# Kernel optimization log

Measured on AMD Instinct MI355X. Metric: run time of the kernel, lower is better.

The kernel has to match this reference:

```python
import jax, jax.numpy as jnp
import numpy as np

N, C, K2 = 40000, 128, 9  # active voxels, channels, 3x3 kernel taps
HEAD_OUT = {"hm": 3, "center": 2, "center_z": 1, "dim": 3, "rot": 2}
EPS = 1e-5
INIT_BIAS = -2.66


def setup_inputs() -> dict:
    key = jax.random.key(0)
    ks = jax.random.split(key, 16)
    feats = jax.random.normal(ks[0], (N, C), dtype=jnp.float32)
    # precomputed submanifold-conv neighbor indices (one per kernel tap, all valid)
    nbr_idx = jax.random.randint(ks[1], (N, K2), 0, N, dtype=jnp.int32)
    H = len(HEAD_OUT)
    inp = {"feats": feats, "nbr_idx": nbr_idx}
    # stacked 3x3 SubMConv weights for all heads (kaiming-ish scale)
    inp["W1"] = jax.random.normal(ks[2], (H, K2, C, C), dtype=jnp.float32) * (2.0 / (K2 * C)) ** 0.5
    inp["gamma"] = jnp.ones((H, C), jnp.float32)
    inp["beta"] = jnp.zeros((H, C), jnp.float32)
    for i, (name, oc) in enumerate(HEAD_OUT.items()):
        inp[f"w_{name}"] = jax.random.normal(ks[3 + i], (C, oc), dtype=jnp.float32) * (2.0 / C) ** 0.5
        inp[f"b_{name}"] = (jnp.full((oc,), INIT_BIAS, jnp.float32) if name == "hm"
                             else jnp.zeros((oc,), jnp.float32))
    return inp


def reference(feats, nbr_idx, W1, gamma, beta,
              w_hm, b_hm, w_center, b_center, w_center_z, b_center_z,
              w_dim, b_dim, w_rot, b_rot):
    # SubMConv2d as gather + contraction over kernel taps (shared by all heads)
    gathered = feats[nbr_idx]                       # [N, K2, C]
    y = jnp.einsum('nkc,hkcd->hnd', gathered, W1)   # [H, N, C]
    # BatchNorm1d (training-mode forward: biased batch stats over voxels) + ReLU
    mean = y.mean(axis=1, keepdims=True)
    var = y.var(axis=1, keepdims=True)
    y = jax.nn.relu((y - mean) * jax.lax.rsqrt(var + EPS) * gamma[:, None, :] + beta[:, None, :])
    # per-head 1x1 SubMConv with bias
    heads = [(w_hm, b_hm), (w_center, b_center), (w_center_z, b_center_z),
             (w_dim, b_dim), (w_rot, b_rot)]
    outs = [y[i] @ w + b for i, (w, b) in enumerate(heads)]
    # concat head outputs along channel: [N, 3+2+1+3+2] = [N, 11]
    return jnp.concatenate(outs, axis=-1)
```

## Files before the change

kernel.cpp:

```cpp
#include <hip/hip_runtime.h>
#include <stdint.h>

#define NVOX 40000
#define CCH  128
#define K2   9
#define NH   5
#define TILES 313

typedef __attribute__((ext_vector_type(8))) short bf16x8;
typedef __attribute__((ext_vector_type(4))) float f32x4;

__device__ __forceinline__ unsigned short f2b(float f) {
  union { float f; unsigned int u; } v; v.f = f;
  return (unsigned short)((v.u + 0x7fffu + ((v.u >> 16) & 1u)) >> 16);
}
__device__ __forceinline__ float b2f(unsigned short u) {
  union { unsigned int u; float f; } v; v.u = ((unsigned int)u) << 16;
  return v.f;
}
__device__ __forceinline__ void g2l16(const void* g, void* l) {
  __builtin_amdgcn_global_load_lds(
      (const __attribute__((address_space(1))) unsigned int*)g,
      (__attribute__((address_space(3))) unsigned int*)l, 16, 0, 0);
}
__device__ __forceinline__ int swz(int row, int col) {
  return row * 128 + ((((col >> 3) ^ (row & 15)) << 3) | (col & 7));
}

__global__ void prep(const float4* __restrict__ feats, ushort4* __restrict__ fb,
                     const float* __restrict__ w1, unsigned short* __restrict__ w1t,
                     float* __restrict__ sums) {
  __shared__ unsigned short t[128 * 34];
  int b = blockIdx.x;
  if (b < 5000) {
    int i = b * 256 + threadIdx.x;
    if (i < NVOX * CCH / 4) {
      float4 v = feats[i];
      ushort4 r;
      r.x = f2b(v.x); r.y = f2b(v.y); r.z = f2b(v.z); r.w = f2b(v.w);
      fb[i] = r;
    }
    return;
  }
  if (b == 5180) {
    for (int i = threadIdx.x; i < 2 * NH * CCH; i += 256) sums[i] = 0.f;
    return;
  }
  int bb = b - 5000;
  int tile = bb >> 2;
  int q = bb & 3;
  const float* src = w1 + (size_t)tile * 16384 + q * 32 * 128;
  for (int e = threadIdx.x; e < 4096; e += 256) {
    int c = e >> 7, d = e & 127;
    t[d * 34 + c] = f2b(src[e]);
  }
  __syncthreads();
  unsigned short* dst = w1t + (size_t)tile * 16384 + q * 32;
  for (int e = threadIdx.x; e < 4096; e += 256) {
    int d = e >> 5, c = e & 31;
    dst[d * 128 + c] = t[d * 34 + c];
  }
}

__device__ __forceinline__ void stageB(unsigned short* dstbuf, const unsigned short* wp,
                                       int wave, int lane) {
  int lcol = lane & 15, lrow = lane >> 4;
#pragma unroll
  for (int i = 0; i < 8; ++i) {
    int elem = wave * 4096 + i * 512;
    int row = (elem >> 7) + lrow;
    g2l16(wp + row * 128 + ((lcol ^ (row & 15)) << 3), &dstbuf[elem]);
  }
}

__global__ void __launch_bounds__(256, 2) conv_gemm(
    const unsigned short* __restrict__ fb,
    const int* __restrict__ nbr,
    const unsigned short* __restrict__ w1t,
    unsigned short* __restrict__ yb,
    float* __restrict__ sums)
{
  __shared__ __align__(16) unsigned short Bsb[2][128 * 128];
  __shared__ int idxs[128 * K2];

  const int bid = blockIdx.x;
  const int s = bid / 40;
  const int r = bid % 40;
  const int h = r >> 3;
  const int x = r & 7;
  const int tile = s * 8 + x;
  if (tile >= TILES) return;
  const int n0 = tile * 128;

  const int tid = threadIdx.x;
  const int wave = tid >> 6;
  const int lane = tid & 63;
  const int m = lane & 15;
  const int quad = lane >> 4;

  const unsigned short* wh = w1t + ((size_t)h * K2 << 14);

  stageB(Bsb[0], wh, wave, lane);

  for (int i = tid; i < 128 * K2; i += 256) {
    int rr = i / K2;
    int gn = n0 + rr; if (gn > NVOX - 1) gn = NVOX - 1;
    idxs[i] = nbr[gn * K2 + (i - rr * K2)];
  }
  __syncthreads();

  bf16x8 A[2][2][4];
  {
    int i0 = idxs[(wave * 32 + m) * K2 + 0];
    int i1 = idxs[(wave * 32 + 16 + m) * K2 + 0];
    const unsigned short* p0 = fb + (size_t)i0 * CCH + quad * 8;
    const unsigned short* p1 = fb + (size_t)i1 * CCH + quad * 8;
#pragma unroll
    for (int kc = 0; kc < 4; ++kc) {
      A[0][0][kc] = *(const bf16x8*)(p0 + kc * 32);
      A[0][1][kc] = *(const bf16x8*)(p1 + kc * 32);
    }
  }

  f32x4 acc[2][8] = {};

#pragma unroll
  for (int k = 0; k < K2; ++k) {
    const int par = k & 1;
    if (k + 1 < K2) {
      stageB(Bsb[par ^ 1], wh + ((size_t)(k + 1) << 14), wave, lane);
      int i0 = idxs[(wave * 32 + m) * K2 + k + 1];
      int i1 = idxs[(wave * 32 + 16 + m) * K2 + k + 1];
      const unsigned short* p0 = fb + (size_t)i0 * CCH + quad * 8;
      const unsigned short* p1 = fb + (size_t)i1 * CCH + quad * 8;
#pragma unroll
      for (int kc = 0; kc < 4; ++kc) {
        A[par ^ 1][0][kc] = *(const bf16x8*)(p0 + kc * 32);
        A[par ^ 1][1][kc] = *(const bf16x8*)(p1 + kc * 32);
      }
    }
    const unsigned short* Bcur = Bsb[par];
#pragma unroll
    for (int kc = 0; kc < 4; ++kc) {
      bf16x8 bfr[8];
#pragma unroll
      for (int ni = 0; ni < 8; ++ni)
        bfr[ni] = *(const bf16x8*)&Bcur[(ni * 16 + m) * CCH + (((kc * 4 + quad) ^ m) << 3)];
#pragma unroll
      for (int ni = 0; ni < 8; ++ni) {
        acc[0][ni] = __builtin_amdgcn_mfma_f32_16x16x32_bf16(A[par][0][kc], bfr[ni], acc[0][ni], 0, 0, 0);
        acc[1][ni] = __builtin_amdgcn_mfma_f32_16x16x32_bf16(A[par][1][kc], bfr[ni], acc[1][ni], 0, 0, 0);
      }
    }
    if (k + 1 < K2) {
      asm volatile("s_waitcnt vmcnt(0)" ::: "memory");
      __syncthreads();
    }
  }

  __syncthreads();
  const bool full = (n0 + 128 <= NVOX);
  unsigned short* epi = (unsigned short*)Bsb[0];
  float2* pb = (float2*)Bsb[1];

#pragma unroll
  for (int mi = 0; mi < 2; ++mi)
#pragma unroll
    for (int ni = 0; ni < 8; ++ni)
#pragma unroll
      for (int rr = 0; rr < 4; ++rr) {
        int row = wave * 32 + mi * 16 + quad * 4 + rr;
        int col = ni * 16 + m;
        epi[swz(row, col)] = f2b(acc[mi][ni][rr]);
      }

#pragma unroll
  for (int ni = 0; ni < 8; ++ni) {
    float sm = 0.f, q = 0.f;
#pragma unroll
    for (int mi = 0; mi < 2; ++mi)
#pragma unroll
      for (int rr = 0; rr < 4; ++rr) {
        float v = acc[mi][ni][rr];
        if (!full && n0 + wave * 32 + mi * 16 + quad * 4 + rr >= NVOX) v = 0.f;
        sm += v; q += v * v;
      }
    pb[(ni * 16 + m) * 17 + wave * 4 + quad] = make_float2(sm, q);
  }
  __syncthreads();

  for (int i = tid; i < 2048; i += 256) {
    int row = i >> 4;
    int c = i & 15;
    if (n0 + row < NVOX)
      *(bf16x8*)(yb + ((size_t)h * NVOX + n0 + row) * CCH + c * 8) =
          *(const bf16x8*)&epi[row * 128 + ((c ^ (row & 15)) << 3)];
  }

  if (tid < 128) {
    float sm = 0.f, q = 0.f;
#pragma unroll
    for (int c = 0; c < 16; ++c) {
      float2 p = pb[tid * 17 + c];
      sm += p.x; q += p.y;
    }
    atomicAdd(&sums[h * CCH + tid], sm);
    atomicAdd(&sums[NH * CCH + h * CCH + tid], q);
  }
}

__global__ void finalize_bn(const float* __restrict__ sums, const float* __restrict__ gamma,
                            const float* __restrict__ beta, float* __restrict__ ssb) {
  int h = blockIdx.x, c = threadIdx.x;
  float mean = sums[h * CCH + c] * (1.f / NVOX);
  float var = sums[NH * CCH + h * CCH + c] * (1.f / NVOX) - mean * mean;
  float rstd = rsqrtf(var + 1e-5f);
  float scale = rstd * gamma[h * CCH + c];
  ssb[h * CCH + c] = scale;
  ssb[NH * CCH + h * CCH + c] = beta[h * CCH + c] - mean * scale;
}

__global__ void __launch_bounds__(256) head_fuse(
    const unsigned short* __restrict__ yb, const float* __restrict__ ssb,
    const float* __restrict__ w_hm, const float* __restrict__ b_hm,
    const float* __restrict__ w_ce, const float* __restrict__ b_ce,
    const float* __restrict__ w_cz, const float* __restrict__ b_cz,
    const float* __restrict__ w_dm, const float* __restrict__ b_dm,
    const float* __restrict__ w_rt, const float* __restrict__ b_rt,
    float* __restrict__ out)
{
  __shared__ unsigned short t[64 * 128];
  __shared__ float pbuf[4][64][12];

  const int tid = threadIdx.x;
  const int v0 = blockIdx.x * 64;
  const int vx = tid & 63;
  const int qd = tid >> 6;

  float part[11];
#pragma unroll
  for (int j = 0; j < 11; ++j) part[j] = 0.f;

#pragma unroll
  for (int h = 0; h < NH; ++h) {
    __syncthreads();
#pragma unroll
    for (int i = 0; i < 4; ++i) {
      int idx = i * 256 + tid;
      int row = idx >> 4, c = idx & 15;
      *(bf16x8*)&t[row * 128 + ((c ^ (row & 15)) << 3)] =
          *(const bf16x8*)(yb + ((size_t)h * NVOX + v0 + row) * CCH + c * 8);
    }
    __syncthreads();

    const float* sc = ssb + h * CCH;
    const float* sh = ssb + NH * CCH + h * CCH;
    const float* wp; int oc, off;
    switch (h) {
      case 0: wp = w_hm; oc = 3; off = 0; break;
      case 1: wp = w_ce; oc = 2; off = 3; break;
      case 2: wp = w_cz; oc = 1; off = 5; break;
      case 3: wp = w_dm; oc = 3; off = 6; break;
      default: wp = w_rt; oc = 2; off = 9; break;
    }
#pragma unroll
    for (int qq = 0; qq < 4; ++qq) {
      int q8 = qd * 4 + qq;
      bf16x8 pk = *(const bf16x8*)&t[vx * 128 + ((q8 ^ (vx & 15)) << 3)];
#pragma unroll
      for (int e = 0; e < 8; ++e) {
        int d = q8 * 8 + e;
        float z = fmaf(b2f((unsigned short)pk[e]), sc[d], sh[d]);
        z = fmaxf(z, 0.f);
        const float* wr = wp + d * oc;
        part[off] = fmaf(z, wr[0], part[off]);
        if (oc > 1) part[off + 1] = fmaf(z, wr[1], part[off + 1]);
        if (oc > 2) part[off + 2] = fmaf(z, wr[2], part[off + 2]);
      }
    }
  }

#pragma unroll
  for (int j = 0; j < 11; ++j) pbuf[qd][vx][j] = part[j];
  __syncthreads();
  if (tid < 64) {
    float o[11];
#pragma unroll
    for (int j = 0; j < 11; ++j)
      o[j] = pbuf[0][tid][j] + pbuf[1][tid][j] + pbuf[2][tid][j] + pbuf[3][tid][j];
    o[0] += b_hm[0]; o[1] += b_hm[1]; o[2] += b_hm[2];
    o[3] += b_ce[0]; o[4] += b_ce[1];
    o[5] += b_cz[0];
    o[6] += b_dm[0]; o[7] += b_dm[1]; o[8] += b_dm[2];
    o[9] += b_rt[0]; o[10] += b_rt[1];
    float* op = out + (size_t)(v0 + tid) * 11;
#pragma unroll
    for (int j = 0; j < 11; ++j) op[j] = o[j];
  }
}

extern "C" void kernel_launch(void* const* d_in, const int* in_sizes, int n_in,
                              void* d_out, int out_size, void* d_ws, size_t ws_size,
                              hipStream_t stream) {
  const float* feats = (const float*)d_in[0];
  const int*   nbr   = (const int*)d_in[1];
  const float* W1    = (const float*)d_in[2];
  const float* gamma = (const float*)d_in[3];
  const float* beta  = (const float*)d_in[4];
  const float* w_hm = (const float*)d_in[5];  const float* b_hm = (const float*)d_in[6];
  const float* w_ce = (const float*)d_in[7];  const float* b_ce = (const float*)d_in[8];
  const float* w_cz = (const float*)d_in[9];  const float* b_cz = (const float*)d_in[10];
  const float* w_dm = (const float*)d_in[11]; const float* b_dm = (const float*)d_in[12];
  const float* w_rt = (const float*)d_in[13]; const float* b_rt = (const float*)d_in[14];
  float* out = (float*)d_out;

  char* ws = (char*)d_ws;
  unsigned short* w1t = (unsigned short*)ws;
  unsigned short* fb  = (unsigned short*)(ws + 11796480);
  unsigned short* yb  = (unsigned short*)(ws + 22036480);
  float* sums = (float*)(ws + 73236480);
  float* ssb  = (float*)(ws + 73241600);

  prep<<<5181, 256, 0, stream>>>((const float4*)feats, (ushort4*)fb, W1, w1t, sums);
  conv_gemm<<<1600, 256, 0, stream>>>(fb, nbr, w1t, yb, sums);
  finalize_bn<<<NH, CCH, 0, stream>>>(sums, gamma, beta, ssb);
  head_fuse<<<625, 256, 0, stream>>>(yb, ssb, w_hm, b_hm, w_ce, b_ce, w_cz, b_cz,
                                     w_dm, b_dm, w_rt, b_rt, out);
}
```

Baseline: 237.1 us.

## Halve conv weight LDS staging for higher occupancy and fold BN finalize into head kernel

```diff
diff --git a/kernel.cpp b/kernel.cpp
--- a/kernel.cpp
+++ b/kernel.cpp
@@ -62,25 +62,26 @@
   }
 }
 
-__device__ __forceinline__ void stageB(unsigned short* dstbuf, const unsigned short* wp,
-                                       int wave, int lane) {
-  int lcol = lane & 15, lrow = lane >> 4;
-#pragma unroll
-  for (int i = 0; i < 8; ++i) {
-    int elem = wave * 4096 + i * 512;
-    int row = (elem >> 7) + lrow;
-    g2l16(wp + row * 128 + ((lcol ^ (row & 15)) << 3), &dstbuf[elem]);
-  }
-}
-
-__global__ void __launch_bounds__(256, 2) conv_gemm(
+__device__ __forceinline__ void stageBhalf(unsigned short* dst, const unsigned short* wp,
+                                           int half, int wave, int lane) {
+  int lrow = lane >> 3;
+  int lch  = lane & 7;
+#pragma unroll
+  for (int i = 0; i < 4; ++i) {
+    int rb = (wave * 4 + i) * 8;
+    g2l16(wp + (rb + lrow) * 128 + half * 64 + ((lch ^ lrow) << 3),
+          &dst[(wave * 4 + i) * 512]);
+  }
+}
+
+__global__ void __launch_bounds__(256, 4) conv_gemm(
     const unsigned short* __restrict__ fb,
     const int* __restrict__ nbr,
     const unsigned short* __restrict__ w1t,
     unsigned short* __restrict__ yb,
     float* __restrict__ sums)
 {
-  __shared__ __align__(16) unsigned short Bsb[2][128 * 128];
+  __shared__ __align__(16) unsigned short Bsb[2][64 * 128];
   __shared__ int idxs[128 * K2];
 
   const int bid = blockIdx.x;
@@ -100,7 +101,7 @@
 
   const unsigned short* wh = w1t + ((size_t)h * K2 << 14);
 
-  stageB(Bsb[0], wh, wave, lane);
+  stageBhalf(Bsb[0], wh, 0, wave, lane);
 
   for (int i = tid; i < 128 * K2; i += 256) {
     int rr = i / K2;
@@ -121,14 +122,17 @@
       A[0][1][kc] = *(const bf16x8*)(p1 + kc * 32);
     }
   }
+  asm volatile("s_waitcnt vmcnt(0)" ::: "memory");
+  __syncthreads();
 
   f32x4 acc[2][8] = {};
 
 #pragma unroll
   for (int k = 0; k < K2; ++k) {
     const int par = k & 1;
+
+    stageBhalf(Bsb[1], wh + ((size_t)k << 14), 1, wave, lane);
     if (k + 1 < K2) {
-      stageB(Bsb[par ^ 1], wh + ((size_t)(k + 1) << 14), wave, lane);
       int i0 = idxs[(wave * 32 + m) * K2 + k + 1];
       int i1 = idxs[(wave * 32 + 16 + m) * K2 + k + 1];
       const unsigned short* p0 = fb + (size_t)i0 * CCH + quad * 8;
@@ -139,29 +143,41 @@
         A[par ^ 1][1][kc] = *(const bf16x8*)(p1 + kc * 32);
       }
     }
-    const unsigned short* Bcur = Bsb[par];
-#pragma unroll
-    for (int kc = 0; kc < 4; ++kc) {
+#pragma unroll
+    for (int kc = 0; kc < 2; ++kc) {
       bf16x8 bfr[8];
 #pragma unroll
       for (int ni = 0; ni < 8; ++ni)
-        bfr[ni] = *(const bf16x8*)&Bcur[(ni * 16 + m) * CCH + (((kc * 4 + quad) ^ m) << 3)];
+        bfr[ni] = *(const bf16x8*)&Bsb[0][(ni * 16 + m) * 64 + ((((kc & 1) * 4 + quad) ^ (m & 7)) << 3)];
 #pragma unroll
       for (int ni = 0; ni < 8; ++ni) {
         acc[0][ni] = __builtin_amdgcn_mfma_f32_16x16x32_bf16(A[par][0][kc], bfr[ni], acc[0][ni], 0, 0, 0);
         acc[1][ni] = __builtin_amdgcn_mfma_f32_16x16x32_bf16(A[par][1][kc], bfr[ni], acc[1][ni], 0, 0, 0);
       }
     }
-    if (k + 1 < K2) {
-      asm volatile("s_waitcnt vmcnt(0)" ::: "memory");
-      __syncthreads();
-    }
-  }
-
-  __syncthreads();
+    asm volatile("s_waitcnt vmcnt(0)" ::: "memory");
+    __syncthreads();
+
+    if (k + 1 < K2)
+      stageBhalf(Bsb[0], wh + ((size_t)(k + 1) << 14), 0, wave, lane);
+#pragma unroll
+    for (int kc = 2; kc < 4; ++kc) {
+      bf16x8 bfr[8];
+#pragma unroll
+      for (int ni = 0; ni < 8; ++ni)
+        bfr[ni] = *(const bf16x8*)&Bsb[1][(ni * 16 + m) * 64 + ((((kc & 1) * 4 + quad) ^ (m & 7)) << 3)];
+#pragma unroll
+      for (int ni = 0; ni < 8; ++ni) {
+        acc[0][ni] = __builtin_amdgcn_mfma_f32_16x16x32_bf16(A[par][0][kc], bfr[ni], acc[0][ni], 0, 0, 0);
+        acc[1][ni] = __builtin_amdgcn_mfma_f32_16x16x32_bf16(A[par][1][kc], bfr[ni], acc[1][ni], 0, 0, 0);
+      }
+    }
+    asm volatile("s_waitcnt vmcnt(0)" ::: "memory");
+    __syncthreads();
+  }
+
   const bool full = (n0 + 128 <= NVOX);
-  unsigned short* epi = (unsigned short*)Bsb[0];
-  float2* pb = (float2*)Bsb[1];
+  unsigned short* epi = &Bsb[0][0];
 
 #pragma unroll
   for (int mi = 0; mi < 2; ++mi)
@@ -174,6 +190,7 @@
         epi[swz(row, col)] = f2b(acc[mi][ni][rr]);
       }
 
+  float psm[8], pq[8];
 #pragma unroll
   for (int ni = 0; ni < 8; ++ni) {
     float sm = 0.f, q = 0.f;
@@ -185,7 +202,7 @@
         if (!full && n0 + wave * 32 + mi * 16 + quad * 4 + rr >= NVOX) v = 0.f;
         sm += v; q += v * v;
       }
-    pb[(ni * 16 + m) * 17 + wave * 4 + quad] = make_float2(sm, q);
+    psm[ni] = sm; pq[ni] = q;
   }
   __syncthreads();
 
@@ -196,6 +213,13 @@
       *(bf16x8*)(yb + ((size_t)h * NVOX + n0 + row) * CCH + c * 8) =
           *(const bf16x8*)&epi[row * 128 + ((c ^ (row & 15)) << 3)];
   }
+  __syncthreads();
+
+  float2* pb = (float2*)&Bsb[0][0];
+#pragma unroll
+  for (int ni = 0; ni < 8; ++ni)
+    pb[(ni * 16 + m) * 17 + wave * 4 + quad] = make_float2(psm[ni], pq[ni]);
+  __syncthreads();
 
   if (tid < 128) {
     float sm = 0.f, q = 0.f;
@@ -209,19 +233,9 @@
   }
 }
 
-__global__ void finalize_bn(const float* __restrict__ sums, const float* __restrict__ gamma,
-                            const float* __restrict__ beta, float* __restrict__ ssb) {
-  int h = blockIdx.x, c = threadIdx.x;
-  float mean = sums[h * CCH + c] * (1.f / NVOX);
-  float var = sums[NH * CCH + h * CCH + c] * (1.f / NVOX) - mean * mean;
-  float rstd = rsqrtf(var + 1e-5f);
-  float scale = rstd * gamma[h * CCH + c];
-  ssb[h * CCH + c] = scale;
-  ssb[NH * CCH + h * CCH + c] = beta[h * CCH + c] - mean * scale;
-}
-
 __global__ void __launch_bounds__(256) head_fuse(
-    const unsigned short* __restrict__ yb, const float* __restrict__ ssb,
+    const unsigned short* __restrict__ yb, const float* __restrict__ sums,
+    const float* __restrict__ gamma, const float* __restrict__ beta,
     const float* __restrict__ w_hm, const float* __restrict__ b_hm,
     const float* __restrict__ w_ce, const float* __restrict__ b_ce,
     const float* __restrict__ w_cz, const float* __restrict__ b_cz,
@@ -231,11 +245,21 @@
 {
   __shared__ unsigned short t[64 * 128];
   __shared__ float pbuf[4][64][12];
+  __shared__ float scl[NH * CCH], shf[NH * CCH];
 
   const int tid = threadIdx.x;
   const int v0 = blockIdx.x * 64;
   const int vx = tid & 63;
   const int qd = tid >> 6;
+
+  for (int i = tid; i < NH * CCH; i += 256) {
+    float mean = sums[i] * (1.f / NVOX);
+    float var = sums[NH * CCH + i] * (1.f / NVOX) - mean * mean;
+    float rstd = rsqrtf(var + 1e-5f);
+    float sc = rstd * gamma[i];
+    scl[i] = sc;
+    shf[i] = beta[i] - mean * sc;
+  }
 
   float part[11];
 #pragma unroll
@@ -253,8 +277,8 @@
     }
     __syncthreads();
 
-    const float* sc = ssb + h * CCH;
-    const float* sh = ssb + NH * CCH + h * CCH;
+    const float* sc = scl + h * CCH;
+    const float* sh = shf + h * CCH;
     const float* wp; int oc, off;
     switch (h) {
       case 0: wp = w_hm; oc = 3; off = 0; break;
@@ -319,11 +343,9 @@
   unsigned short* fb  = (unsigned short*)(ws + 11796480);
   unsigned short* yb  = (unsigned short*)(ws + 22036480);
   float* sums = (float*)(ws + 73236480);
-  float* ssb  = (float*)(ws + 73241600);
 
   prep<<<5181, 256, 0, stream>>>((const float4*)feats, (ushort4*)fb, W1, w1t, sums);
   conv_gemm<<<1600, 256, 0, stream>>>(fb, nbr, w1t, yb, sums);
-  finalize_bn<<<NH, CCH, 0, stream>>>(sums, gamma, beta, ssb);
-  head_fuse<<<625, 256, 0, stream>>>(yb, ssb, w_hm, b_hm, w_ce, b_ce, w_cz, b_cz,
-                                     w_dm, b_dm, w_rt, b_rt, out);
-}
+  head_fuse<<<625, 256, 0, stream>>>(yb, sums, gamma, beta, w_hm, b_hm, w_ce, b_ce,
+                                     w_cz, b_cz, w_dm, b_dm, w_rt, b_rt, out);
+}
```

Result: slower. 259.4 us (+9.4%).
